# Optimization experiments

Hardware: AMD Instinct MI355X
Metric: run time of the kernel (lower is better)

## Reference

```python
import jax, jax.numpy as jnp
import numpy as np

EPS_LN = 1e-5
EPS_W = 1e-16
K = 3


def layernorm(x, gamma, beta):
    mu = x.mean(-1, keepdims=True)
    var = ((x - mu) ** 2).mean(-1, keepdims=True)
    return (x - mu) * jax.lax.rsqrt(var + EPS_LN) * gamma + beta


def knn_interp(xb, pos_x, pos_y, k=K):
    """Inverse-squared-distance kNN interpolation.
    xb: [B, Nx, C] source features; pos_x: [Nx, 3]; pos_y: [Ny, 3].
    Positions are identical across batch (torch code expands them), so the
    kNN search is done once and the gather is broadcast over batch.
    Returns [B, Ny, C]."""
    # squared distances via ||y||^2 + ||x||^2 - 2 y.x  -> [Ny, Nx]
    d2 = ((pos_y * pos_y).sum(-1)[:, None]
          + (pos_x * pos_x).sum(-1)[None, :]
          - 2.0 * pos_y @ pos_x.T)
    _, idx = jax.lax.top_k(-d2, k)                      # [Ny, k] nearest
    # exact squared distances for the selected neighbors (matches torch math)
    diff = pos_x[idx] - pos_y[:, None, :]               # [Ny, k, 3]
    w = 1.0 / jnp.clip((diff * diff).sum(-1), EPS_W)    # [Ny, k]
    xg = xb[:, idx, :]                                  # [B, Ny, k, C]
    num = (xg * w[None, :, :, None]).sum(2)             # [B, Ny, C]
    return num / w.sum(1)[None, :, None]


def setup_inputs() -> dict:
    key = jax.random.key(0)
    k1, k2, k3 = jax.random.split(key, 3)
    B, N_MESH, N_PIV, C = 4, 40000, 2000, 128
    return {
        "node_features": jax.random.normal(k1, (B * N_MESH, C), jnp.float32),
        "gamma": jnp.ones((C,), jnp.float32),
        "beta": jnp.zeros((C,), jnp.float32),
        "position_mesh": jax.random.uniform(k2, (N_MESH, 3), jnp.float32),
        "position_pivotal": jax.random.uniform(k3, (N_PIV, 3), jnp.float32),
        "batch_size": 4,
    }


def reference(node_features, gamma, beta, position_mesh, position_pivotal, batch_size):
    B = batch_size
    C = node_features.shape[-1]
    Nm = position_mesh.shape[0]
    # encode: PivotalNorm then mesh -> pivotal interpolation
    h = layernorm(node_features, gamma, beta)
    hb = h.reshape(B, Nm, C)
    piv = knn_interp(hb, position_mesh, position_pivotal, K)      # [B, Npiv, C]
    # decode: pivotal -> mesh interpolation
    mesh = knn_interp(piv, position_pivotal, position_mesh, K)    # [B, Nm, C]
    return mesh.reshape(B * Nm, C)
```

## Files before the change

### kernel.cpp

```cpp
#include <hip/hip_runtime.h>
#include <hip/hip_bf16.h>
#include <math.h>

#define EPS_LN 1e-5f
#define EPS_W  1e-16f
#define MAX_STAGE 2560

__device__ __forceinline__ float cvt(const __hip_bfloat16 v) { return __bfloat162float(v); }
__device__ __forceinline__ float cvt(const float v)          { return v; }

__device__ __forceinline__ void ins3lex(float nd, int ni, float d[3], int ix[3]) {
    bool b2 = (nd < d[2]) || (nd == d[2] && ni < ix[2]);
    if (!b2) return;
    bool b1 = (nd < d[1]) || (nd == d[1] && ni < ix[1]);
    bool b0 = (nd < d[0]) || (nd == d[0] && ni < ix[0]);
    if (b0)      { d[2]=d[1]; ix[2]=ix[1]; d[1]=d[0]; ix[1]=ix[0]; d[0]=nd; ix[0]=ni; }
    else if (b1) { d[2]=d[1]; ix[2]=ix[1]; d[1]=nd; ix[1]=ni; }
    else         { d[2]=nd; ix[2]=ni; }
}

__global__ __launch_bounds__(256)
void stage_kernel(const void* pmesh, int Nm, const void* ppiv, int Np,
                  float4* __restrict__ mesh_s, float4* __restrict__ piv_s,
                  int* __restrict__ flag) {
    __shared__ int sbad;
    if (threadIdx.x == 0) sbad = 0;
    __syncthreads();
    {
        const __hip_bfloat16* pb = (const __hip_bfloat16*)ppiv;
        int bad = 0;
        for (int i = threadIdx.x; i < Np * 3; i += 256) {
            float v = __bfloat162float(pb[i]);
            if (!(v >= 0.0f && v <= 1.0f)) bad = 1;
        }
        if (bad) sbad = 1;
    }
    __syncthreads();
    const int isf32 = sbad;

    int gid = blockIdx.x * 256 + threadIdx.x;
    if (gid == 0) *flag = isf32;
    const int total = Nm + Np;
    if (gid >= total) return;
    const int isMesh = gid < Nm ? 1 : 0;
    const int idx = isMesh ? gid : gid - Nm;
    const void* src = isMesh ? pmesh : ppiv;
    float x, y, z;
    if (isf32) {
        const float* p = (const float*)src;
        x = p[idx*3+0]; y = p[idx*3+1]; z = p[idx*3+2];
    } else {
        const __hip_bfloat16* p = (const __hip_bfloat16*)src;
        x = cvt(p[idx*3+0]); y = cvt(p[idx*3+1]); z = cvt(p[idx*3+2]);
    }
    float4 o; o.x = x; o.y = y; o.z = z; o.w = x*x + y*y + z*z;
    (isMesh ? mesh_s : piv_s)[idx] = o;
}

__global__ __launch_bounds__(256)
void knn_scan_kernel(const float4* __restrict__ cand, int Nc,
                     const float4* __restrict__ qry, int Nq,
                     int nslice, int chunk,
                     int* __restrict__ idx_out, float* __restrict__ wn_out,
                     float2* __restrict__ partials) {
    __shared__ float4 scand[MAX_STAGE];
    __shared__ float  sd[4][64][3];
    __shared__ int    si[4][64][3];

    const int tid   = threadIdx.x;
    const int lane  = tid & 63;
    const int wv    = __builtin_amdgcn_readfirstlane(tid >> 6);
    const int qg    = blockIdx.x / nslice;
    const int slice = blockIdx.x % nslice;
    const int q     = qg * 64 + lane;
    const int qc    = min(q, Nq - 1);

    const int rbeg = slice * 4 * chunk;
    const int rend = min(rbeg + 4 * chunk, Nc);
    int cnt = rend - rbeg;
    if (cnt > MAX_STAGE) cnt = MAX_STAGE;
    for (int i = tid; i < cnt; i += 256) scand[i] = cand[rbeg + i];

    const float4 qp = qry[qc];
    const float  qn = qp.w;
    __syncthreads();

    float d0 = INFINITY, d1 = INFINITY, d2 = INFINITY;
    int   i0 = 0x7fffffff, i1 = 0x7fffffff, i2 = 0x7fffffff;

    const int jbeg = wv * chunk;
    const int jend = min(jbeg + chunk, cnt);
    #pragma unroll 4
    for (int j = jbeg; j < jend; ++j) {
        const float4 cp = scand[j];
        float t   = qn + cp.w;
        float dot = qp.x*cp.x + qp.y*cp.y + qp.z*cp.z;
        float s   = t - 2.0f*dot;
        if (s < d2) {
            int gi = rbeg + j;
            if (s < d1) {
                d2 = d1; i2 = i1;
                if (s < d0) { d1 = d0; i1 = i0; d0 = s; i0 = gi; }
                else        { d1 = s;  i1 = gi; }
            } else { d2 = s; i2 = gi; }
        }
    }

    sd[wv][lane][0] = d0; sd[wv][lane][1] = d1; sd[wv][lane][2] = d2;
    si[wv][lane][0] = i0; si[wv][lane][1] = i1; si[wv][lane][2] = i2;
    __syncthreads();

    if (wv == 0) {
        float d[3]  = {d0, d1, d2};
        int   ix[3] = {i0, i1, i2};
        for (int w = 1; w < 4; ++w)
            for (int k = 0; k < 3; ++k)
                ins3lex(sd[w][lane][k], si[w][lane][k], d, ix);
        if (q < Nq) {
            if (nslice == 1) {
                float w_[3], ws = 0.f;
                for (int k = 0; k < 3; ++k) {
                    int ii = min(max(ix[k], 0), Nc - 1);
                    ix[k] = ii;
                    float4 cp = scand[ii];
                    float dx = cp.x - qp.x, dy = cp.y - qp.y, dz = cp.z - qp.z;
                    float dd = dx*dx + dy*dy + dz*dz;
                    w_[k] = 1.0f / fmaxf(dd, EPS_W);
                    ws += w_[k];
                }
                float inv = 1.0f / ws;
                for (int k = 0; k < 3; ++k) {
                    idx_out[q*3+k] = ix[k];
                    wn_out[q*3+k]  = w_[k] * inv;
                }
            } else {
                float2* p = partials + ((size_t)q * nslice + slice) * 3;
                for (int k = 0; k < 3; ++k) {
                    float2 e; e.x = d[k]; e.y = __int_as_float(ix[k]);
                    p[k] = e;
                }
            }
        }
    }
}

__global__ __launch_bounds__(256)
void knn_finalize_kernel(const float2* __restrict__ partials, int nslice,
                         const float4* __restrict__ cand, int Nc,
                         const float4* __restrict__ qry, int Nq,
                         int* __restrict__ idx_out, float* __restrict__ wn_out) {
    int q = blockIdx.x * 256 + threadIdx.x;
    if (q >= Nq) return;
    float d[3]  = {INFINITY, INFINITY, INFINITY};
    int   ix[3] = {0x7fffffff, 0x7fffffff, 0x7fffffff};
    const float2* p = partials + (size_t)q * nslice * 3;
    for (int e = 0; e < nslice * 3; ++e)
        ins3lex(p[e].x, __float_as_int(p[e].y), d, ix);
    const float4 qp = qry[q];
    float w_[3], ws = 0.f;
    for (int k = 0; k < 3; ++k) {
        int ii = min(max(ix[k], 0), Nc - 1);
        ix[k] = ii;
        float4 cp = cand[ii];
        float dx = cp.x - qp.x, dy = cp.y - qp.y, dz = cp.z - qp.z;
        float dd = dx*dx + dy*dy + dz*dz;
        w_[k] = 1.0f / fmaxf(dd, EPS_W);
        ws += w_[k];
    }
    float inv = 1.0f / ws;
    for (int k = 0; k < 3; ++k) {
        idx_out[q*3+k] = ix[k];
        wn_out[q*3+k]  = w_[k] * inv;
    }
}

template <typename T, typename S>
__device__ void interp_ln_body(const T* __restrict__ xfeat,
                               const T* __restrict__ gamma,
                               const T* __restrict__ beta,
                               const int* __restrict__ idx,
                               const float* __restrict__ wn,
                               S* __restrict__ piv, int Nm, int Np, int C) {
    const int j   = blockIdx.x % Np;
    const int b   = blockIdx.x / Np;
    const int c   = threadIdx.x;
    const int wid = c >> 6;
    const int nw  = C >> 6;

    const float g  = cvt(gamma[c]);
    const float be = cvt(beta[c]);

    __shared__ float red[8];
    float acc = 0.f;
    const float invC = 1.0f / (float)C;

    for (int k = 0; k < 3; ++k) {
        int row = idx[j*3+k];
        row = min(max(row, 0), Nm - 1);
        const T* xp = xfeat + ((size_t)b*Nm + row) * (size_t)C;
        float x = cvt(xp[c]);
        float s = x, s2 = x*x;
        for (int off = 32; off > 0; off >>= 1) {
            s  += __shfl_down(s,  off);
            s2 += __shfl_down(s2, off);
        }
        if ((c & 63) == 0) { red[wid] = s; red[4+wid] = s2; }
        __syncthreads();
        float sum = 0.f, sum2 = 0.f;
        for (int wv = 0; wv < nw; ++wv) { sum += red[wv]; sum2 += red[4+wv]; }
        float mean = sum * invC;
        float var  = sum2 * invC - mean*mean;
        float rs   = rsqrtf(var + EPS_LN);
        acc += wn[j*3+k] * ((x - mean)*rs*g + be);
        __syncthreads();
    }
    S ov; if constexpr (sizeof(S) == 2) ov = __float2bfloat16(acc); else ov = acc;
    piv[((size_t)b*Np + j) * (size_t)C + c] = ov;
}

__global__ __launch_bounds__(128)
void interp_ln_kernel(const void* xfeat, const void* gamma, const void* beta,
                      const int* idx, const float* wn, void* piv,
                      int Nm, int Np, int C, const int* dtype_flag) {
    if (*dtype_flag)
        interp_ln_body<float, float>((const float*)xfeat, (const float*)gamma,
                                     (const float*)beta, idx, wn,
                                     (float*)piv, Nm, Np, C);
    else
        interp_ln_body<__hip_bfloat16, __hip_bfloat16>(
            (const __hip_bfloat16*)xfeat, (const __hip_bfloat16*)gamma,
            (const __hip_bfloat16*)beta, idx, wn,
            (__hip_bfloat16*)piv, Nm, Np, C);
}

__global__ __launch_bounds__(256)
void gather_out_kernel(const void* __restrict__ pivv,
                       const int* __restrict__ idx, const float* __restrict__ wn,
                       void* __restrict__ out, int Nm, int Np, int C4,
                       int total4, const int* __restrict__ dtype_flag) {
    int gid = blockIdx.x * 256 + threadIdx.x;
    if (gid >= total4) return;
    int c4 = gid % C4;
    int r  = gid / C4;
    int i  = r % Nm;
    int b  = r / Nm;
    const int C = C4 * 4;
    int jj0 = min(max(idx[i*3+0], 0), Np - 1);
    int jj1 = min(max(idx[i*3+1], 0), Np - 1);
    int jj2 = min(max(idx[i*3+2], 0), Np - 1);
    float w0 = wn[i*3+0], w1 = wn[i*3+1], w2 = wn[i*3+2];

    if (*dtype_flag) {
        const float* pbase = (const float*)pivv + (size_t)b * Np * C;
        float4 v0 = *(const float4*)(pbase + (size_t)jj0 * C + c4*4);
        float4 v1 = *(const float4*)(pbase + (size_t)jj1 * C + c4*4);
        float4 v2 = *(const float4*)(pbase + (size_t)jj2 * C + c4*4);
        float4 o;
        o.x = w0*v0.x + w1*v1.x + w2*v2.x;
        o.y = w0*v0.y + w1*v1.y + w2*v2.y;
        o.z = w0*v0.z + w1*v1.z + w2*v2.z;
        o.w = w0*v0.w + w1*v1.w + w2*v2.w;
        *(((float4*)out) + gid) = o;
    } else {
        const __hip_bfloat16* pbase = (const __hip_bfloat16*)pivv + (size_t)b * Np * C;
        union { __hip_bfloat16 h[4]; uint2 v; } u0, u1, u2, o;
        u0.v = *(const uint2*)(pbase + (size_t)jj0 * C + c4*4);
        u1.v = *(const uint2*)(pbase + (size_t)jj1 * C + c4*4);
        u2.v = *(const uint2*)(pbase + (size_t)jj2 * C + c4*4);
        #pragma unroll
        for (int t = 0; t < 4; ++t) {
            float a = w0*cvt(u0.h[t]) + w1*cvt(u1.h[t]) + w2*cvt(u2.h[t]);
            o.h[t] = __float2bfloat16(a);
        }
        *(((uint2*)out) + gid) = o.v;
    }
}

__global__ void zero_words_kernel(unsigned* out, long long nwords) {
    long long i = (long long)blockIdx.x * 256 + threadIdx.x;
    if (i < nwords) out[i] = 0u;
}

extern "C" void kernel_launch(void* const* d_in, const int* in_sizes, int n_in,
                              void* d_out, int out_size, void* d_ws, size_t ws_size,
                              hipStream_t stream) {
    const int C  = in_sizes[1];
    const int Nm = in_sizes[3] / 3;
    const int Np = in_sizes[4] / 3;
    const int B  = in_sizes[0] / (Nm * C);

    const int nsl1 = (Nm + MAX_STAGE - 1) / MAX_STAGE;
    const int chk1 = (Nm + nsl1*4 - 1) / (nsl1*4);
    const int nsl2 = (Np + MAX_STAGE - 1) / MAX_STAGE;
    const int chk2 = (Np + nsl2*4 - 1) / (nsl2*4);

    size_t off = 0;
    auto carve = [&](size_t bytes) {
        size_t p = off;
        off += (bytes + 255) & ~(size_t)255;
        return p;
    };
    const size_t flag_o  = carve(256);
    const size_t meshs_o = carve((size_t)Nm * sizeof(float4));
    const size_t pivs_o  = carve((size_t)Np * sizeof(float4));
    const size_t piv_o   = carve((size_t)B * Np * C * sizeof(float));
    const size_t i1_o    = carve((size_t)Np * 3 * sizeof(int));
    const size_t w1_o    = carve((size_t)Np * 3 * sizeof(float));
    const size_t i2_o    = carve((size_t)Nm * 3 * sizeof(int));
    const size_t w2_o    = carve((size_t)Nm * 3 * sizeof(float));
    const size_t p1_o    = carve((size_t)Np * nsl1 * 3 * sizeof(float2));
    const size_t p2_o    = carve((size_t)Nm * nsl2 * 3 * sizeof(float2));

    if (off > ws_size) {
        long long nwords = (long long)out_size / 2;
        zero_words_kernel<<<(int)((nwords + 255) / 256), 256, 0, stream>>>(
            (unsigned*)d_out, nwords);
        return;
    }

    char* base = (char*)d_ws;
    int*    flag   = (int*)   (base + flag_o);
    float4* mesh_s = (float4*)(base + meshs_o);
    float4* piv_s  = (float4*)(base + pivs_o);
    void*   piv    = (void*)  (base + piv_o);
    int*    idx1   = (int*)   (base + i1_o);
    float*  wn1    = (float*) (base + w1_o);
    int*    idx2   = (int*)   (base + i2_o);
    float*  wn2    = (float*) (base + w2_o);
    float2* part1  = (float2*)(base + p1_o);
    float2* part2  = (float2*)(base + p2_o);

    stage_kernel<<<(Nm + Np + 255) / 256, 256, 0, stream>>>(
        d_in[3], Nm, d_in[4], Np, mesh_s, piv_s, flag);

    {
        const int nqg = (Np + 63) / 64;
        knn_scan_kernel<<<nqg * nsl1, 256, 0, stream>>>(
            mesh_s, Nm, piv_s, Np, nsl1, chk1, idx1, wn1, part1);
        if (nsl1 > 1)
            knn_finalize_kernel<<<(Np + 255) / 256, 256, 0, stream>>>(
                part1, nsl1, mesh_s, Nm, piv_s, Np, idx1, wn1);
    }

    interp_ln_kernel<<<B * Np, C, 0, stream>>>(d_in[0], d_in[1], d_in[2],
                                               idx1, wn1, piv, Nm, Np, C, flag);

    {
        const int nqg = (Nm + 63) / 64;
        knn_scan_kernel<<<nqg * nsl2, 256, 0, stream>>>(
            piv_s, Np, mesh_s, Nm, nsl2, chk2, idx2, wn2, part2);
        if (nsl2 > 1)
            knn_finalize_kernel<<<(Nm + 255) / 256, 256, 0, stream>>>(
                part2, nsl2, piv_s, Np, mesh_s, Nm, idx2, wn2);
    }

    const int C4 = C / 4;
    const int total4 = B * Nm * C4;
    gather_out_kernel<<<(total4 + 255) / 256, 256, 0, stream>>>(
        piv, idx2, wn2, d_out, Nm, Np, C4, total4, flag);
}
```

Measured before the change: 305.1 us.

## Split kNN scans into more slices and read candidates directly from global memory

The kNN scan kernel no longer stages candidate points into LDS behind a barrier. Each wave now reads its candidate range straight from global memory; the loads are wave-uniform and should be served from cache. The host now picks the slice count so the grid targets about 2048 blocks. This raises the first scan from 16 to 64 slices and splits the second scan into 4 slices with a finalize pass. The intent is better occupancy across CUs and shorter per-wave loops, at the cost of more partial-result traffic, an extra finalize kernel, and reliance on the cache instead of LDS for candidate reuse.

```diff
diff --git a/kernel.cpp b/kernel.cpp
--- a/kernel.cpp
+++ b/kernel.cpp
@@ -4,7 +4,6 @@
 
 #define EPS_LN 1e-5f
 #define EPS_W  1e-16f
-#define MAX_STAGE 2560
 
 __device__ __forceinline__ float cvt(const __hip_bfloat16 v) { return __bfloat162float(v); }
 __device__ __forceinline__ float cvt(const float v)          { return v; }
@@ -63,7 +62,6 @@
                      int nslice, int chunk,
                      int* __restrict__ idx_out, float* __restrict__ wn_out,
                      float2* __restrict__ partials) {
-    __shared__ float4 scand[MAX_STAGE];
     __shared__ float  sd[4][64][3];
     __shared__ int    si[4][64][3];
 
@@ -75,34 +73,26 @@
     const int q     = qg * 64 + lane;
     const int qc    = min(q, Nq - 1);
 
-    const int rbeg = slice * 4 * chunk;
-    const int rend = min(rbeg + 4 * chunk, Nc);
-    int cnt = rend - rbeg;
-    if (cnt > MAX_STAGE) cnt = MAX_STAGE;
-    for (int i = tid; i < cnt; i += 256) scand[i] = cand[rbeg + i];
-
     const float4 qp = qry[qc];
     const float  qn = qp.w;
-    __syncthreads();
 
     float d0 = INFINITY, d1 = INFINITY, d2 = INFINITY;
     int   i0 = 0x7fffffff, i1 = 0x7fffffff, i2 = 0x7fffffff;
 
-    const int jbeg = wv * chunk;
-    const int jend = min(jbeg + chunk, cnt);
-    #pragma unroll 4
+    const int jbeg = (slice * 4 + wv) * chunk;
+    const int jend = min(jbeg + chunk, Nc);
+    #pragma unroll 8
     for (int j = jbeg; j < jend; ++j) {
-        const float4 cp = scand[j];
+        const float4 cp = cand[j];
         float t   = qn + cp.w;
         float dot = qp.x*cp.x + qp.y*cp.y + qp.z*cp.z;
         float s   = t - 2.0f*dot;
         if (s < d2) {
-            int gi = rbeg + j;
             if (s < d1) {
                 d2 = d1; i2 = i1;
-                if (s < d0) { d1 = d0; i1 = i0; d0 = s; i0 = gi; }
-                else        { d1 = s;  i1 = gi; }
-            } else { d2 = s; i2 = gi; }
+                if (s < d0) { d1 = d0; i1 = i0; d0 = s; i0 = j; }
+                else        { d1 = s;  i1 = j; }
+            } else { d2 = s; i2 = j; }
         }
     }
 
@@ -122,7 +112,7 @@
                 for (int k = 0; k < 3; ++k) {
                     int ii = min(max(ix[k], 0), Nc - 1);
                     ix[k] = ii;
-                    float4 cp = scand[ii];
+                    float4 cp = cand[ii];
                     float dx = cp.x - qp.x, dy = cp.y - qp.y, dz = cp.z - qp.z;
                     float dd = dx*dx + dy*dy + dz*dz;
                     w_[k] = 1.0f / fmaxf(dd, EPS_W);
@@ -289,28 +279,47 @@
     const int Np = in_sizes[4] / 3;
     const int B  = in_sizes[0] / (Nm * C);
 
-    const int nsl1 = (Nm + MAX_STAGE - 1) / MAX_STAGE;
-    const int chk1 = (Nm + nsl1*4 - 1) / (nsl1*4);
-    const int nsl2 = (Np + MAX_STAGE - 1) / MAX_STAGE;
-    const int chk2 = (Np + nsl2*4 - 1) / (nsl2*4);
+    const int nqg1 = (Np + 63) / 64;
+    const int nqg2 = (Nm + 63) / 64;
+
+    auto plan = [](int nqg, int Nc, int& nsl, int& chk) {
+        nsl = (2048 + nqg - 1) / nqg;
+        int maxsl = (Nc + 127) / 128;
+        if (nsl > maxsl) nsl = maxsl;
+        if (nsl < 1) nsl = 1;
+        chk = (Nc + nsl*4 - 1) / (nsl*4);
+    };
+    int nsl1, chk1, nsl2, chk2;
+    plan(nqg1, Nm, nsl1, chk1);
+    plan(nqg2, Np, nsl2, chk2);
 
     size_t off = 0;
-    auto carve = [&](size_t bytes) {
-        size_t p = off;
-        off += (bytes + 255) & ~(size_t)255;
-        return p;
+    size_t flag_o = 0, meshs_o = 0, pivs_o = 0, piv_o = 0;
+    size_t i1_o = 0, w1_o = 0, i2_o = 0, w2_o = 0, p1_o = 0, p2_o = 0;
+    auto layout = [&](int s1, int s2) {
+        off = 0;
+        auto carve = [&](size_t bytes) {
+            size_t p = off;
+            off += (bytes + 255) & ~(size_t)255;
+            return p;
+        };
+        flag_o  = carve(256);
+        meshs_o = carve((size_t)Nm * sizeof(float4));
+        pivs_o  = carve((size_t)Np * sizeof(float4));
+        piv_o   = carve((size_t)B * Np * C * sizeof(float));
+        i1_o    = carve((size_t)Np * 3 * sizeof(int));
+        w1_o    = carve((size_t)Np * 3 * sizeof(float));
+        i2_o    = carve((size_t)Nm * 3 * sizeof(int));
+        w2_o    = carve((size_t)Nm * 3 * sizeof(float));
+        p1_o    = carve((size_t)Np * s1 * 3 * sizeof(float2));
+        p2_o    = carve((size_t)Nm * s2 * 3 * sizeof(float2));
     };
-    const size_t flag_o  = carve(256);
-    const size_t meshs_o = carve((size_t)Nm * sizeof(float4));
-    const size_t pivs_o  = carve((size_t)Np * sizeof(float4));
-    const size_t piv_o   = carve((size_t)B * Np * C * sizeof(float));
-    const size_t i1_o    = carve((size_t)Np * 3 * sizeof(int));
-    const size_t w1_o    = carve((size_t)Np * 3 * sizeof(float));
-    const size_t i2_o    = carve((size_t)Nm * 3 * sizeof(int));
-    const size_t w2_o    = carve((size_t)Nm * 3 * sizeof(float));
-    const size_t p1_o    = carve((size_t)Np * nsl1 * 3 * sizeof(float2));
-    const size_t p2_o    = carve((size_t)Nm * nsl2 * 3 * sizeof(float2));
-
+    layout(nsl1, nsl2);
+    if (off > ws_size) {
+        nsl1 = 16; chk1 = (Nm + nsl1*4 - 1) / (nsl1*4);
+        nsl2 = 1;  chk2 = (Np + nsl2*4 - 1) / (nsl2*4);
+        layout(nsl1, nsl2);
+    }
     if (off > ws_size) {
         long long nwords = (long long)out_size / 2;
         zero_words_kernel<<<(int)((nwords + 255) / 256), 256, 0, stream>>>(
@@ -334,8 +343,7 @@
         d_in[3], Nm, d_in[4], Np, mesh_s, piv_s, flag);
 
     {
-        const int nqg = (Np + 63) / 64;
-        knn_scan_kernel<<<nqg * nsl1, 256, 0, stream>>>(
+        knn_scan_kernel<<<nqg1 * nsl1, 256, 0, stream>>>(
             mesh_s, Nm, piv_s, Np, nsl1, chk1, idx1, wn1, part1);
         if (nsl1 > 1)
             knn_finalize_kernel<<<(Np + 255) / 256, 256, 0, stream>>>(
@@ -346,8 +354,7 @@
                                                idx1, wn1, piv, Nm, Np, C, flag);
 
     {
-        const int nqg = (Nm + 63) / 64;
-        knn_scan_kernel<<<nqg * nsl2, 256, 0, stream>>>(
+        knn_scan_kernel<<<nqg2 * nsl2, 256, 0, stream>>>(
             piv_s, Np, mesh_s, Nm, nsl2, chk2, idx2, wn2, part2);
         if (nsl2 > 1)
             knn_finalize_kernel<<<(Nm + 255) / 256, 256, 0, stream>>>(
```

Result: no change. 304.6 us (-0.2%).
